# Kernel optimization log

Measured on AMD Instinct MI355X. Metric: run time of the kernel, lower is better.

Reference implementation:

```python
import jax, jax.numpy as jnp
import numpy as np

WS = 7            # window size
HEADS = 4
DIM = 128         # hidden_dim
HEAD_DIM = 128    # wrapper passes head_dim=hidden_dim (faithful to source)
INNER = HEADS * HEAD_DIM   # 512
MLP = 4 * DIM
PATCH = 4
DISP = WS // 2
NEG = -1e9


def _ln(x, g, b, eps=1e-5):
    m = jnp.mean(x, -1, keepdims=True)
    v = jnp.mean((x - m) ** 2, -1, keepdims=True)
    return (x - m) * jax.lax.rsqrt(v + eps) * g + b


_coords = np.stack(np.meshgrid(np.arange(WS), np.arange(WS), indexing='ij'), -1).reshape(-1, 2)
REL_IDX = jnp.asarray(_coords[None] - _coords[:, None] + WS - 1)  # (ws^2, ws^2, 2)


def _build_masks():
    n = WS * WS
    ul = np.zeros((n, n), np.float32)
    ul[-DISP * WS:, : -DISP * WS] = NEG
    ul[: -DISP * WS, -DISP * WS:] = NEG
    lr = np.zeros((WS, WS, WS, WS), np.float32)
    lr[:, -DISP:, :, : -DISP] = NEG
    lr[:, : -DISP, :, -DISP:] = NEG
    return jnp.asarray(ul), jnp.asarray(lr.reshape(n, n))

UL_MASK, LR_MASK = _build_masks()


def _win_attn(x, w_qkv, pos, w_o, b_o, shifted):
    b, H, W, _ = x.shape
    if shifted:
        x = jnp.roll(x, (-DISP, -DISP), axis=(1, 2))
    nh, nw = H // WS, W // WS
    qkv = x @ w_qkv  # (b, H, W, 3*INNER)

    def to_win(t):  # -> (b, heads, n_windows, ws*ws, head_dim)
        t = t.reshape(b, nh, WS, nw, WS, HEADS, HEAD_DIM)
        return t.transpose(0, 5, 1, 3, 2, 4, 6).reshape(b, HEADS, nh * nw, WS * WS, HEAD_DIM)

    q, k, v = map(to_win, jnp.split(qkv, 3, axis=-1))
    dots = jnp.einsum('bhwid,bhwjd->bhwij', q, k) * (HEAD_DIM ** -0.5)
    dots = dots + pos[REL_IDX[..., 0], REL_IDX[..., 1]]  # shared across heads (berniwal)
    if shifted:
        dots = dots.at[:, :, -nw:].add(UL_MASK)
        dots = dots.at[:, :, nw - 1::nw].add(LR_MASK)
    attn = jax.nn.softmax(dots, axis=-1)
    out = jnp.einsum('bhwij,bhwjd->bhwid', attn, v)
    out = out.reshape(b, HEADS, nh, nw, WS, WS, HEAD_DIM).transpose(0, 2, 4, 3, 5, 1, 6)
    out = out.reshape(b, H, W, INNER) @ w_o + b_o
    if shifted:
        out = jnp.roll(out, (DISP, DISP), axis=(1, 2))
    return out


def _block(x, ga1, be1, w_qkv, pos, w_o, b_o, ga2, be2, w1, b1, w2, b2, shifted):
    x = x + _win_attn(_ln(x, ga1, be1), w_qkv, pos, w_o, b_o, shifted)
    h = jax.nn.gelu(_ln(x, ga2, be2) @ w1 + b1, approximate=False) @ w2 + b2
    return x + h


def _patch_embed(x, w, b):  # Unfold(patch) + Linear, channel-major feature order
    B, C, H, W = x.shape
    nh, nw = H // PATCH, W // PATCH
    x = x.reshape(B, C, nh, PATCH, nw, PATCH).transpose(0, 2, 4, 1, 3, 5)
    return x.reshape(B, nh, nw, C * PATCH * PATCH) @ w + b


def setup_inputs() -> dict:
    key = jax.random.key(0)
    ks = iter(jax.random.split(key, 48))

    def nrm(shape, s=0.02):
        return jax.random.normal(next(ks), shape, dtype=jnp.float32) * s

    inp = {'x': jax.random.normal(next(ks), (32, 3, 224, 224), dtype=jnp.float32)}
    inp['w_pe'] = nrm((3 * PATCH * PATCH, DIM))
    inp['b_pe'] = jnp.zeros((DIM,), jnp.float32)
    for s in ('a', 'b'):
        inp['ga1_' + s] = jnp.ones((DIM,), jnp.float32)
        inp['be1_' + s] = jnp.zeros((DIM,), jnp.float32)
        inp['w_qkv_' + s] = nrm((DIM, 3 * INNER))
        inp['pos_' + s] = nrm((2 * WS - 1, 2 * WS - 1), 1.0)
        inp['w_o_' + s] = nrm((INNER, DIM))
        inp['b_o_' + s] = jnp.zeros((DIM,), jnp.float32)
        inp['ga2_' + s] = jnp.ones((DIM,), jnp.float32)
        inp['be2_' + s] = jnp.zeros((DIM,), jnp.float32)
        inp['w_m1_' + s] = nrm((DIM, MLP))
        inp['b_m1_' + s] = jnp.zeros((MLP,), jnp.float32)
        inp['w_m2_' + s] = nrm((MLP, DIM))
        inp['b_m2_' + s] = jnp.zeros((DIM,), jnp.float32)
    return inp


def reference(x, w_pe, b_pe,
              ga1_a, be1_a, w_qkv_a, pos_a, w_o_a, b_o_a, ga2_a, be2_a, w_m1_a, b_m1_a, w_m2_a, b_m2_a,
              ga1_b, be1_b, w_qkv_b, pos_b, w_o_b, b_o_b, ga2_b, be2_b, w_m1_b, b_m1_b, w_m2_b, b_m2_b):
    h = _patch_embed(x, w_pe, b_pe)  # (B, 56, 56, DIM)
    h = _block(h, ga1_a, be1_a, w_qkv_a, pos_a, w_o_a, b_o_a, ga2_a, be2_a, w_m1_a, b_m1_a, w_m2_a, b_m2_a, False)
    h = _block(h, ga1_b, be1_b, w_qkv_b, pos_b, w_o_b, b_o_b, ga2_b, be2_b, w_m1_b, b_m1_b, w_m2_b, b_m2_b, True)
    return h
```

## Files before the change

kernel.cpp:

```cpp
#include <hip/hip_runtime.h>

typedef __attribute__((ext_vector_type(8))) short bf16x8;
typedef __attribute__((ext_vector_type(4))) short bf16x4;
typedef __attribute__((ext_vector_type(4))) float f32x4;
typedef __attribute__((ext_vector_type(2))) unsigned u32x2;

#define MFMA16(a, b, c) __builtin_amdgcn_mfma_f32_16x16x32_bf16(a, b, c, 0, 0, 0)

static __device__ __forceinline__ short f2bf(float f) {
    union { float f; unsigned u; } x; x.f = f;
    unsigned r = x.u + 0x7FFFu + ((x.u >> 16) & 1u);
    return (short)(r >> 16);
}

static __device__ __forceinline__ unsigned cvtpk(float lo, float hi) {
    unsigned r;
    asm("v_cvt_pk_bf16_f32 %0, %1, %2" : "=v"(r) : "v"(lo), "v"(hi));
    return r;
}

static __device__ __forceinline__ void gload16(const void* g, void* l) {
    __builtin_amdgcn_global_load_lds((const __attribute__((address_space(1))) void*)g,
                                     (__attribute__((address_space(3))) void*)l, 16, 0, 0);
}

static __device__ __forceinline__ float gelu(float t) {
    return 0.5f * t * (1.f + erff(t * 0.70710678118f));
}

__global__ void wconv_kernel(const float* __restrict__ i_qkv, const float* __restrict__ i_o,
                             const float* __restrict__ i_m1, const float* __restrict__ i_m2,
                             short* __restrict__ wqkv, short* __restrict__ wo,
                             short* __restrict__ wm1, short* __restrict__ wm2) {
    int idx = blockIdx.x * 256 + threadIdx.x;
    if (idx < 196608) {
        int k = idx & 127, n = idx >> 7;
        wqkv[idx] = f2bf(i_qkv[k * 1536 + n]);
    } else if (idx < 262144) {
        int l = idx - 196608; int k = l & 511, n = l >> 9;
        wo[l] = f2bf(i_o[k * 128 + n]);
    } else if (idx < 327680) {
        int l = idx - 262144; int k = l & 127, n = l >> 7;
        wm1[l] = f2bf(i_m1[k * 512 + n]);
    } else {
        int l = idx - 327680; int k = l & 511, n = l >> 9;
        wm2[l] = f2bf(i_m2[k * 128 + n]);
    }
}

__global__ __launch_bounds__(128) void mtgen_kernel(const float* __restrict__ wqkv,
                                                    short* __restrict__ mt) {
    const int h = blockIdx.x >> 7, e = blockIdx.x & 127;
    __shared__ float s_wk[128];
    const int d = threadIdx.x;
    s_wk[d] = wqkv[(size_t)e * 1536 + 512 + h * 128 + d];
    __syncthreads();
    const float* wq = wqkv + (size_t)d * 1536 + h * 128;
    float acc = 0.f;
#pragma unroll
    for (int o = 0; o < 128; ++o) acc += wq[o] * s_wk[o];
    mt[(size_t)(h * 128 + e) * 128 + d] = f2bf(acc * 0.08838834764831845f);
}

__global__ void tabgen_kernel(const float* __restrict__ pos_a, const float* __restrict__ pos_b,
                              float* __restrict__ tab) {
    int v = blockIdx.x;
    const float* pos = (v == 0) ? pos_a : pos_b;
    for (int e = threadIdx.x; e < 4096; e += 256) {
        int row = e >> 6, key = e & 63;
        float val;
        if (key >= 49) val = -1e9f;
        else if (row >= 49) val = 0.f;
        else {
            int qi = row / 7, qj = row - qi * 7, ki = key / 7, kj = key - ki * 7;
            val = pos[(ki - qi + 6) * 13 + (kj - qj + 6)];
            if (v >= 1) {
                bool wh7 = (v - 1) & 2, ww7 = (v - 1) & 1;
                if (wh7 && ((qi >= 4) != (ki >= 4))) val += -1e9f;
                if (ww7 && ((qj >= 4) != (kj >= 4))) val += -1e9f;
            }
        }
        tab[v * 4096 + e] = val;
    }
}

__global__ __launch_bounds__(256) void patchln_kernel(const float* __restrict__ x,
                                                      const float* __restrict__ w,
                                                      const float* __restrict__ bias,
                                                      const float* __restrict__ g,
                                                      const float* __restrict__ bta,
                                                      float* __restrict__ out,
                                                      short* __restrict__ xn) {
    __shared__ float s_in[2][48];
    __shared__ float red[2][2][2];
    const int tid = threadIdx.x;
    const int half = tid >> 7, c = tid & 127;
    const int winh = (tid >> 6) & 1, lane = tid & 63;
    const int t = blockIdx.x * 2 + half;
    const int b = t / 3136, rem = t - b * 3136;
    const int hp = rem / 56, wp = rem - hp * 56;
    if (c < 48) {
        int cin = c >> 4, py = (c >> 2) & 3, px = c & 3;
        s_in[half][c] = x[((size_t)(b * 3 + cin) * 224 + hp * 4 + py) * 224 + wp * 4 + px];
    }
    __syncthreads();
    float acc = bias[c];
#pragma unroll
    for (int k = 0; k < 48; ++k) acc += s_in[half][k] * w[k * 128 + c];
    out[(size_t)t * 128 + c] = acc;
    float s1 = acc, s2 = acc * acc;
#pragma unroll
    for (int o = 32; o > 0; o >>= 1) { s1 += __shfl_xor(s1, o); s2 += __shfl_xor(s2, o); }
    if (lane == 0) { red[half][winh][0] = s1; red[half][winh][1] = s2; }
    __syncthreads();
    s1 = red[half][0][0] + red[half][1][0];
    s2 = red[half][0][1] + red[half][1][1];
    float mean = s1 * (1.f / 128.f);
    float var = s2 * (1.f / 128.f) - mean * mean;
    float rstd = rsqrtf(var + 1e-5f);
    xn[(size_t)t * 128 + c] = f2bf((acc - mean) * rstd * g[c] + bta[c]);
}

template <int SHIFTED>
__global__ __launch_bounds__(256, 3) void attn_kernel(const short* __restrict__ xn,
                                                      const short* __restrict__ wqkvT,
                                                      const short* __restrict__ mt,
                                                      const float* __restrict__ tab,
                                                      const short* __restrict__ zpad,
                                                      short* __restrict__ aout) {
    __shared__ short smem[24576];
    short* s_x = smem;
    short* s_T = smem + 8192;
    short* s_v = smem + 16384;
    short* s_p = smem;

    const int tid = threadIdx.x;
    const int wid = tid >> 6, lane = tid & 63;
    const int l15 = lane & 15, l4 = lane >> 4, klo = l4 * 8;
    const int bid = blockIdx.x;
    const int win = bid & 63, head = (bid >> 6) & 3, b = bid >> 8;
    const int wh = win >> 3, ww = win & 7;

#pragma unroll
    for (int it = 0; it < 4; ++it) {
        int slot = it * 256 + tid;
        int row = slot >> 4, scol = slot & 15;
        int colb = (scol * 16) ^ ((row & 7) << 4);
        const char* g;
        if (row < 49) {
            int wi = (row * 37) >> 8, wj = row - wi * 7;
            int hh = wh * 7 + wi, wp = ww * 7 + wj;
            if (SHIFTED) { hh += 3; if (hh >= 56) hh -= 56; wp += 3; if (wp >= 56) wp -= 56; }
            int t = (b * 56 + hh) * 56 + wp;
            g = (const char*)(xn + (size_t)t * 128) + colb;
        } else {
            g = (const char*)zpad + colb;
        }
        gload16(g, (char*)smem + (it * 256 + wid * 64) * 16);
    }
    __syncthreads();

    const f32x4 zero4 = {0.f, 0.f, 0.f, 0.f};

    {
        const short* Mh = mt + (size_t)head * 16384;
        const short* Wv = wqkvT + (size_t)(1024 + head * 128) * 128;
        f32x4 at[2][4], av[4][2];
#pragma unroll
        for (int mw = 0; mw < 2; ++mw)
#pragma unroll
            for (int j = 0; j < 4; ++j) at[mw][j] = zero4;
#pragma unroll
        for (int m = 0; m < 4; ++m)
#pragma unroll
            for (int n = 0; n < 2; ++n) av[m][n] = zero4;
#pragma unroll
        for (int k0 = 0; k0 < 4; ++k0) {
            bf16x8 bx[4], awt[2], bwv[2];
#pragma unroll
            for (int j = 0; j < 4; ++j) {
                int row = j * 16 + l15;
                bx[j] = *(const bf16x8*)((const char*)s_x + row * 256 + ((k0 * 64 + l4 * 16) ^ ((row & 7) << 4)));
            }
#pragma unroll
            for (int mw = 0; mw < 2; ++mw)
                awt[mw] = *(const bf16x8*)(Mh + (size_t)(wid * 32 + mw * 16 + l15) * 128 + k0 * 32 + klo);
#pragma unroll
            for (int n = 0; n < 2; ++n)
                bwv[n] = *(const bf16x8*)(Wv + (size_t)(wid * 32 + n * 16 + l15) * 128 + k0 * 32 + klo);
            __builtin_amdgcn_s_setprio(1);
#pragma unroll
            for (int mw = 0; mw < 2; ++mw)
#pragma unroll
                for (int j = 0; j < 4; ++j) at[mw][j] = MFMA16(awt[mw], bx[j], at[mw][j]);
#pragma unroll
            for (int m = 0; m < 4; ++m)
#pragma unroll
                for (int n = 0; n < 2; ++n) av[m][n] = MFMA16(bx[m], bwv[n], av[m][n]);
            __builtin_amdgcn_s_setprio(0);
        }
#pragma unroll
        for (int mw = 0; mw < 2; ++mw)
#pragma unroll
            for (int j = 0; j < 4; ++j) {
                u32x2 pq = { cvtpk(at[mw][j][0], at[mw][j][1]), cvtpk(at[mw][j][2], at[mw][j][3]) };
                int row = j * 16 + l15;
                *(u32x2*)((char*)s_T + row * 256 + ((wid * 64 + mw * 32 + l4 * 8) ^ ((row & 7) << 4))) = pq;
            }
#pragma unroll
        for (int m = 0; m < 4; ++m)
#pragma unroll
            for (int n = 0; n < 2; ++n) {
                u32x2 pv = { cvtpk(av[m][n][0], av[m][n][1]), cvtpk(av[m][n][2], av[m][n][3]) };
                int hd = wid * 32 + n * 16 + l15;
                *(u32x2*)((char*)s_v + hd * 128 + ((m * 32 + l4 * 8) ^ ((hd & 7) << 4))) = pv;
            }
    }
    __syncthreads();

    const int qrow = wid * 16 + l15;
    f32x4 dt[4];
#pragma unroll
    for (int m = 0; m < 4; ++m) dt[m] = zero4;
#pragma unroll
    for (int k0 = 0; k0 < 4; ++k0) {
        bf16x8 bq = *(const bf16x8*)((const char*)s_T + qrow * 256 + ((k0 * 64 + l4 * 16) ^ ((qrow & 7) << 4)));
        __builtin_amdgcn_s_setprio(1);
#pragma unroll
        for (int m = 0; m < 4; ++m) {
            int krow = m * 16 + l15;
            bf16x8 akf = *(const bf16x8*)((const char*)s_x + krow * 256 + ((k0 * 64 + l4 * 16) ^ ((krow & 7) << 4)));
            dt[m] = MFMA16(akf, bq, dt[m]);
        }
        __builtin_amdgcn_s_setprio(0);
    }
    __syncthreads();

    const int variant = SHIFTED ? (1 + ((wh == 7) ? 2 : 0) + ((ww == 7) ? 1 : 0)) : 0;
    const float* tv = tab + variant * 4096 + qrow * 64;
    float p[4][4];
    float mx = -3.0e38f;
#pragma unroll
    for (int m = 0; m < 4; ++m) {
        f32x4 tb = *(const f32x4*)(tv + m * 16 + l4 * 4);
#pragma unroll
        for (int r = 0; r < 4; ++r) {
            float d = dt[m][r] + tb[r];
            p[m][r] = d;
            mx = fmaxf(mx, d);
        }
    }
    mx = fmaxf(mx, __shfl_xor(mx, 16));
    mx = fmaxf(mx, __shfl_xor(mx, 32));
    float sum = 0.f;
#pragma unroll
    for (int m = 0; m < 4; ++m)
#pragma unroll
        for (int r = 0; r < 4; ++r) { p[m][r] = __expf(p[m][r] - mx); sum += p[m][r]; }
    sum += __shfl_xor(sum, 16);
    sum += __shfl_xor(sum, 32);
    float inv = 1.f / sum;
#pragma unroll
    for (int m = 0; m < 4; ++m) {
        u32x2 pv = { cvtpk(p[m][0] * inv, p[m][1] * inv), cvtpk(p[m][2] * inv, p[m][3] * inv) };
        *(u32x2*)((char*)s_p + qrow * 128 + ((m * 32 + l4 * 8) ^ ((qrow & 7) << 4))) = pv;
    }
    __syncthreads();

    f32x4 o[4][2];
#pragma unroll
    for (int m = 0; m < 4; ++m)
#pragma unroll
        for (int n = 0; n < 2; ++n) o[m][n] = zero4;
#pragma unroll
    for (int k0 = 0; k0 < 2; ++k0) {
        bf16x8 ap[4], bv[2];
#pragma unroll
        for (int m = 0; m < 4; ++m) {
            int row = m * 16 + l15;
            ap[m] = *(const bf16x8*)((const char*)s_p + row * 128 + ((k0 * 64 + l4 * 16) ^ ((row & 7) << 4)));
        }
#pragma unroll
        for (int n = 0; n < 2; ++n) {
            int hd = wid * 32 + n * 16 + l15;
            bv[n] = *(const bf16x8*)((const char*)s_v + hd * 128 + ((k0 * 64 + l4 * 16) ^ ((hd & 7) << 4)));
        }
        __builtin_amdgcn_s_setprio(1);
#pragma unroll
        for (int m = 0; m < 4; ++m)
#pragma unroll
            for (int n = 0; n < 2; ++n) o[m][n] = MFMA16(ap[m], bv[n], o[m][n]);
        __builtin_amdgcn_s_setprio(0);
    }
#pragma unroll
    for (int m = 0; m < 4; ++m) {
#pragma unroll
        for (int r = 0; r < 4; ++r) {
            int rl = m * 16 + l4 * 4 + r;
            if (rl < 49) {
                int wi = (rl * 37) >> 8, wj = rl - wi * 7;
                int hh = wh * 7 + wi, wp = ww * 7 + wj;
                if (SHIFTED) { hh += 3; if (hh >= 56) hh -= 56; wp += 3; if (wp >= 56) wp -= 56; }
                size_t t = (size_t)(b * 56 + hh) * 56 + wp;
                aout[t * 512 + head * 128 + wid * 32 + l15] = f2bf(o[m][0][r]);
                aout[t * 512 + head * 128 + wid * 32 + 16 + l15] = f2bf(o[m][1][r]);
            }
        }
    }
}

__global__ __launch_bounds__(256, 2) void projmlp_kernel(const short* __restrict__ A,
                                                         const short* __restrict__ woT,
                                                         const short* __restrict__ wm1T,
                                                         const float* __restrict__ b_o,
                                                         const float* __restrict__ ga2,
                                                         const float* __restrict__ be2,
                                                         const float* __restrict__ b1,
                                                         float* __restrict__ outf,
                                                         short* __restrict__ hid) {
    __shared__ char smem[65536];
    float* red = (float*)(smem + 32768);

    const int tid = threadIdx.x, wid = tid >> 6, lane = tid & 63;
    const int wr = wid >> 1, wc = wid & 1;
    const int l15 = lane & 15, l4 = lane >> 4;
    const int m0 = blockIdx.x * 128;

    auto stage = [&](int kc, int bi) {
#pragma unroll
        for (int it = 0; it < 4; ++it) {
            int slot = it * 256 + tid;
            int row = slot >> 3, scol = slot & 7;
            int colb = (scol * 16) ^ ((row & 7) << 4);
            gload16((const char*)(A + (size_t)(m0 + row) * 512 + kc * 64) + colb,
                    (char*)smem + bi * 32768 + (it * 256 + wid * 64) * 16);
        }
#pragma unroll
        for (int it = 0; it < 4; ++it) {
            int slot = it * 256 + tid;
            int row = slot >> 3, scol = slot & 7;
            int colb = (scol * 16) ^ ((row & 7) << 4);
            gload16((const char*)(woT + (size_t)row * 512 + kc * 64) + colb,
                    (char*)smem + bi * 32768 + 16384 + (it * 256 + wid * 64) * 16);
        }
    };

    const f32x4 zero4 = {0.f, 0.f, 0.f, 0.f};
    f32x4 acc[4][4];
#pragma unroll
    for (int nf = 0; nf < 4; ++nf)
#pragma unroll
        for (int tm = 0; tm < 4; ++tm) acc[nf][tm] = zero4;

    stage(0, 0);
    __syncthreads();
#pragma unroll
    for (int kc = 0; kc < 8; ++kc) {
        if (kc + 1 < 8) stage(kc + 1, (kc + 1) & 1);
        const char* bufA = (const char*)smem + (kc & 1) * 32768;
        const char* bufB = bufA + 16384;
#pragma unroll
        for (int ks = 0; ks < 2; ++ks) {
            bf16x8 a[4], bfr[4];
#pragma unroll
            for (int tm = 0; tm < 4; ++tm) {
                int row = wr * 64 + tm * 16 + l15;
                a[tm] = *(const bf16x8*)(bufA + row * 128 + ((ks * 64 + l4 * 16) ^ ((row & 7) << 4)));
            }
#pragma unroll
            for (int nf = 0; nf < 4; ++nf) {
                int row = wc * 64 + nf * 16 + l15;
                bfr[nf] = *(const bf16x8*)(bufB + row * 128 + ((ks * 64 + l4 * 16) ^ ((row & 7) << 4)));
            }
            __builtin_amdgcn_s_setprio(1);
#pragma unroll
            for (int nf = 0; nf < 4; ++nf)
#pragma unroll
                for (int tm = 0; tm < 4; ++tm) acc[nf][tm] = MFMA16(bfr[nf], a[tm], acc[nf][tm]);
            __builtin_amdgcn_s_setprio(0);
        }
        __syncthreads();
    }

    f32x4 bv4[4];
#pragma unroll
    for (int nf = 0; nf < 4; ++nf)
        bv4[nf] = *(const f32x4*)(b_o + wc * 64 + nf * 16 + l4 * 4);

    float s1[4], s2[4];
#pragma unroll
    for (int tm = 0; tm < 4; ++tm) {
        int row = m0 + wr * 64 + tm * 16 + l15;
        float a1 = 0.f, a2 = 0.f;
#pragma unroll
        for (int nf = 0; nf < 4; ++nf) {
            f32x4 rs = *(const f32x4*)(outf + (size_t)row * 128 + wc * 64 + nf * 16 + l4 * 4);
#pragma unroll
            for (int r = 0; r < 4; ++r) {
                float v = acc[nf][tm][r] + bv4[nf][r] + rs[r];
                acc[nf][tm][r] = v;
                a1 += v; a2 += v * v;
            }
        }
        s1[tm] = a1; s2[tm] = a2;
    }
#pragma unroll
    for (int tm = 0; tm < 4; ++tm) {
        s1[tm] += __shfl_xor(s1[tm], 16); s1[tm] += __shfl_xor(s1[tm], 32);
        s2[tm] += __shfl_xor(s2[tm], 16); s2[tm] += __shfl_xor(s2[tm], 32);
    }
    if (l4 == 0) {
#pragma unroll
        for (int tm = 0; tm < 4; ++tm) {
            int lrow = wr * 64 + tm * 16 + l15;
            red[lrow * 4 + wc * 2] = s1[tm];
            red[lrow * 4 + wc * 2 + 1] = s2[tm];
        }
    }
    __syncthreads();

    float mean[4], rstd[4];
#pragma unroll
    for (int tm = 0; tm < 4; ++tm) {
        int lrow = wr * 64 + tm * 16 + l15;
        f32x4 rd = *(const f32x4*)(red + lrow * 4);
        float t1 = rd[0] + rd[2], t2 = rd[1] + rd[3];
        mean[tm] = t1 * (1.f / 128.f);
        float var = t2 * (1.f / 128.f) - mean[tm] * mean[tm];
        rstd[tm] = rsqrtf(var + 1e-5f);
    }
    __syncthreads();

#pragma unroll
    for (int tm = 0; tm < 4; ++tm) {
        int lrow = wr * 64 + tm * 16 + l15;
        int row = m0 + lrow;
#pragma unroll
        for (int nf = 0; nf < 4; ++nf) {
            int col0 = wc * 64 + nf * 16 + l4 * 4;
            *(f32x4*)(outf + (size_t)row * 128 + col0) = acc[nf][tm];
            f32x4 gg = *(const f32x4*)(ga2 + col0);
            f32x4 bb = *(const f32x4*)(be2 + col0);
            float w0 = (acc[nf][tm][0] - mean[tm]) * rstd[tm] * gg[0] + bb[0];
            float w1 = (acc[nf][tm][1] - mean[tm]) * rstd[tm] * gg[1] + bb[1];
            float w2 = (acc[nf][tm][2] - mean[tm]) * rstd[tm] * gg[2] + bb[2];
            float w3 = (acc[nf][tm][3] - mean[tm]) * rstd[tm] * gg[3] + bb[3];
            u32x2 pb = { cvtpk(w0, w1), cvtpk(w2, w3) };
            *(u32x2*)((char*)smem + lrow * 256 + ((col0 * 2) ^ ((lrow & 7) << 4))) = pb;
        }
    }
    __syncthreads();

    for (int hc = 0; hc < 4; ++hc) {
#pragma unroll
        for (int it = 0; it < 8; ++it) {
            int slot = it * 256 + tid;
            int row = slot >> 4, scol = slot & 15;
            int colb = (scol * 16) ^ ((row & 7) << 4);
            gload16((const char*)(wm1T + (size_t)(hc * 128 + row) * 128) + colb,
                    (char*)smem + 32768 + (it * 256 + wid * 64) * 16);
        }
        __syncthreads();

        f32x4 acc2[4][4];
#pragma unroll
        for (int nf = 0; nf < 4; ++nf)
#pragma unroll
            for (int tm = 0; tm < 4; ++tm) acc2[nf][tm] = zero4;
#pragma unroll
        for (int ks = 0; ks < 4; ++ks) {
            bf16x8 a[4], bfr[4];
#pragma unroll
            for (int tm = 0; tm < 4; ++tm) {
                int row = wr * 64 + tm * 16 + l15;
                a[tm] = *(const bf16x8*)((const char*)smem + row * 256 + ((ks * 64 + l4 * 16) ^ ((row & 7) << 4)));
            }
#pragma unroll
            for (int nf = 0; nf < 4; ++nf) {
                int hrow = wc * 64 + nf * 16 + l15;
                bfr[nf] = *(const bf16x8*)((const char*)smem + 32768 + hrow * 256 + ((ks * 64 + l4 * 16) ^ ((hrow & 7) << 4)));
            }
            __builtin_amdgcn_s_setprio(1);
#pragma unroll
            for (int nf = 0; nf < 4; ++nf)
#pragma unroll
                for (int tm = 0; tm < 4; ++tm) acc2[nf][tm] = MFMA16(bfr[nf], a[tm], acc2[nf][tm]);
            __builtin_amdgcn_s_setprio(0);
        }

        f32x4 b14[4];
#pragma unroll
        for (int nf = 0; nf < 4; ++nf)
            b14[nf] = *(const f32x4*)(b1 + hc * 128 + wc * 64 + nf * 16 + l4 * 4);
#pragma unroll
        for (int tm = 0; tm < 4; ++tm) {
            int row = m0 + wr * 64 + tm * 16 + l15;
#pragma unroll
            for (int nf = 0; nf < 4; ++nf) {
                float v0 = gelu(acc2[nf][tm][0] + b14[nf][0]);
                float v1 = gelu(acc2[nf][tm][1] + b14[nf][1]);
                float v2 = gelu(acc2[nf][tm][2] + b14[nf][2]);
                float v3 = gelu(acc2[nf][tm][3] + b14[nf][3]);
                u32x2 pv = { cvtpk(v0, v1), cvtpk(v2, v3) };
                *(u32x2*)(hid + (size_t)row * 512 + hc * 128 + wc * 64 + nf * 16 + l4 * 4) = pv;
            }
        }
        __syncthreads();
    }
}

template <int MODE>
__global__ __launch_bounds__(256, 2) void gemm4_kernel(const short* __restrict__ A,
                                                       const short* __restrict__ BT,
                                                       const float* __restrict__ bias,
                                                       const float* __restrict__ g,
                                                       const float* __restrict__ bta,
                                                       float* __restrict__ outf,
                                                       short* __restrict__ outb) {
    __shared__ char smem[65536];
    float* red = (float*)smem;

    const int tid = threadIdx.x, wid = tid >> 6, lane = tid & 63;
    const int wr = wid >> 1, wc = wid & 1;
    const int l15 = lane & 15, l4 = lane >> 4;
    const int m0 = blockIdx.x * 128;

    auto stage = [&](int kc, int bi) {
#pragma unroll
        for (int it = 0; it < 4; ++it) {
            int slot = it * 256 + tid;
            int row = slot >> 3, scol = slot & 7;
            int colb = (scol * 16) ^ ((row & 7) << 4);
            gload16((const char*)(A + (size_t)(m0 + row) * 512 + kc * 64) + colb,
                    (char*)smem + bi * 32768 + (it * 256 + wid * 64) * 16);
        }
#pragma unroll
        for (int it = 0; it < 4; ++it) {
            int slot = it * 256 + tid;
            int row = slot >> 3, scol = slot & 7;
            int colb = (scol * 16) ^ ((row & 7) << 4);
            gload16((const char*)(BT + (size_t)row * 512 + kc * 64) + colb,
                    (char*)smem + bi * 32768 + 16384 + (it * 256 + wid * 64) * 16);
        }
    };

    const f32x4 zero4 = {0.f, 0.f, 0.f, 0.f};
    f32x4 acc[4][4];
#pragma unroll
    for (int nf = 0; nf < 4; ++nf)
#pragma unroll
        for (int tm = 0; tm < 4; ++tm) acc[nf][tm] = zero4;

    stage(0, 0);
    __syncthreads();
#pragma unroll
    for (int kc = 0; kc < 8; ++kc) {
        if (kc + 1 < 8) stage(kc + 1, (kc + 1) & 1);
        const char* bufA = (const char*)smem + (kc & 1) * 32768;
        const char* bufB = bufA + 16384;
#pragma unroll
        for (int ks = 0; ks < 2; ++ks) {
            bf16x8 a[4], bfr[4];
#pragma unroll
            for (int tm = 0; tm < 4; ++tm) {
                int row = wr * 64 + tm * 16 + l15;
                a[tm] = *(const bf16x8*)(bufA + row * 128 + ((ks * 64 + l4 * 16) ^ ((row & 7) << 4)));
            }
#pragma unroll
            for (int nf = 0; nf < 4; ++nf) {
                int row = wc * 64 + nf * 16 + l15;
                bfr[nf] = *(const bf16x8*)(bufB + row * 128 + ((ks * 64 + l4 * 16) ^ ((row & 7) << 4)));
            }
            __builtin_amdgcn_s_setprio(1);
#pragma unroll
            for (int nf = 0; nf < 4; ++nf)
#pragma unroll
                for (int tm = 0; tm < 4; ++tm) acc[nf][tm] = MFMA16(bfr[nf], a[tm], acc[nf][tm]);
            __builtin_amdgcn_s_setprio(0);
        }
        __syncthreads();
    }

    f32x4 bv4[4];
#pragma unroll
    for (int nf = 0; nf < 4; ++nf)
        bv4[nf] = *(const f32x4*)(bias + wc * 64 + nf * 16 + l4 * 4);

    float s1[4], s2[4];
#pragma unroll
    for (int tm = 0; tm < 4; ++tm) {
        int row = m0 + wr * 64 + tm * 16 + l15;
        float a1 = 0.f, a2 = 0.f;
#pragma unroll
        for (int nf = 0; nf < 4; ++nf) {
            f32x4 rs = *(const f32x4*)(outf + (size_t)row * 128 + wc * 64 + nf * 16 + l4 * 4);
#pragma unroll
            for (int r = 0; r < 4; ++r) {
                float v = acc[nf][tm][r] + bv4[nf][r] + rs[r];
                acc[nf][tm][r] = v;
                a1 += v; a2 += v * v;
            }
        }
        s1[tm] = a1; s2[tm] = a2;
    }

    if (MODE == 1) {
#pragma unroll
        for (int tm = 0; tm < 4; ++tm) {
            s1[tm] += __shfl_xor(s1[tm], 16); s1[tm] += __shfl_xor(s1[tm], 32);
            s2[tm] += __shfl_xor(s2[tm], 16); s2[tm] += __shfl_xor(s2[tm], 32);
        }
        if (l4 == 0) {
#pragma unroll
            for (int tm = 0; tm < 4; ++tm) {
                int lrow = wr * 64 + tm * 16 + l15;
                red[lrow * 4 + wc * 2] = s1[tm];
                red[lrow * 4 + wc * 2 + 1] = s2[tm];
            }
        }
        __syncthreads();
    }

#pragma unroll
    for (int tm = 0; tm < 4; ++tm) {
        int lrow = wr * 64 + tm * 16 + l15;
        int row = m0 + lrow;
        float mean = 0.f, rstd = 0.f;
        if (MODE == 1) {
            f32x4 rd = *(const f32x4*)(red + lrow * 4);
            float t1 = rd[0] + rd[2], t2 = rd[1] + rd[3];
            mean = t1 * (1.f / 128.f);
            float var = t2 * (1.f / 128.f) - mean * mean;
            rstd = rsqrtf(var + 1e-5f);
        }
#pragma unroll
        for (int nf = 0; nf < 4; ++nf) {
            int col0 = wc * 64 + nf * 16 + l4 * 4;
            *(f32x4*)(outf + (size_t)row * 128 + col0) = acc[nf][tm];
            if (MODE == 1) {
                f32x4 gg = *(const f32x4*)(g + col0);
                f32x4 bb = *(const f32x4*)(bta + col0);
                float w0 = (acc[nf][tm][0] - mean) * rstd * gg[0] + bb[0];
                float w1 = (acc[nf][tm][1] - mean) * rstd * gg[1] + bb[1];
                float w2 = (acc[nf][tm][2] - mean) * rstd * gg[2] + bb[2];
                float w3 = (acc[nf][tm][3] - mean) * rstd * gg[3] + bb[3];
                u32x2 pb = { cvtpk(w0, w1), cvtpk(w2, w3) };
                *(u32x2*)(outb + (size_t)row * 128 + col0) = pb;
            }
        }
    }
}

extern "C" void kernel_launch(void* const* d_in, const int* in_sizes, int n_in,
                              void* d_out, int out_size, void* d_ws, size_t ws_size,
                              hipStream_t stream) {
    const float* x = (const float*)d_in[0];
    const float* w_pe = (const float*)d_in[1];
    const float* b_pe = (const float*)d_in[2];
    const float* P[24];
    for (int i = 0; i < 24; ++i) P[i] = (const float*)d_in[3 + i];

    float* out = (float*)d_out;
    const size_t TOK = 100352;

    short* xn = (short*)d_ws;
    short* abuf = xn + TOK * 128;
    short* wqkv = abuf + TOK * 512;
    short* wo = wqkv + 196608;
    short* wm1 = wo + 65536;
    short* wm2 = wm1 + 65536;
    short* mtb = wm2 + 65536;
    float* tab = (float*)(mtb + 65536);
    short* zpad = (short*)(tab + 5 * 4096);

    hipMemsetAsync(zpad, 0, 256, stream);
    tabgen_kernel<<<5, 256, 0, stream>>>(P[3], P[15], tab);

    patchln_kernel<<<50176, 256, 0, stream>>>(x, w_pe, b_pe, P[0], P[1], out, xn);

    for (int s = 0; s < 2; ++s) {
        wconv_kernel<<<1536, 256, 0, stream>>>(P[s * 12 + 2], P[s * 12 + 4], P[s * 12 + 8], P[s * 12 + 10],
                                               wqkv, wo, wm1, wm2);
        mtgen_kernel<<<512, 128, 0, stream>>>(P[s * 12 + 2], mtb);

        if (s == 0)
            attn_kernel<0><<<8192, 256, 0, stream>>>(xn, wqkv, mtb, tab, zpad, abuf);
        else
            attn_kernel<1><<<8192, 256, 0, stream>>>(xn, wqkv, mtb, tab, zpad, abuf);

        projmlp_kernel<<<784, 256, 0, stream>>>(
            abuf, wo, wm1, P[s * 12 + 5], P[s * 12 + 6], P[s * 12 + 7], P[s * 12 + 9], out, abuf);

        if (s == 0)
            gemm4_kernel<1><<<784, 256, 0, stream>>>(
                abuf, wm2, P[11], P[12], P[13], out, xn);
        else
            gemm4_kernel<2><<<784, 256, 0, stream>>>(
                abuf, wm2, P[23], nullptr, nullptr, out, nullptr);
    }
}
```

Before: 549.9 us.

## Vectorize attention output stores, clamp pad rows, load gemm4 weights directly from global

```diff
diff --git a/kernel.cpp b/kernel.cpp
--- a/kernel.cpp
+++ b/kernel.cpp
@@ -126,7 +126,6 @@
                                                       const short* __restrict__ wqkvT,
                                                       const short* __restrict__ mt,
                                                       const float* __restrict__ tab,
-                                                      const short* __restrict__ zpad,
                                                       short* __restrict__ aout) {
     __shared__ short smem[24576];
     short* s_x = smem;
@@ -141,22 +140,28 @@
     const int win = bid & 63, head = (bid >> 6) & 3, b = bid >> 8;
     const int wh = win >> 3, ww = win & 7;
 
+    int trow[4];
+#pragma unroll
+    for (int j = 0; j < 4; ++j) {
+        int r = j * 16 + l15; r = (r > 48) ? 48 : r;
+        int wi = (r * 37) >> 8, wj = r - wi * 7;
+        int hh = wh * 7 + wi, wp = ww * 7 + wj;
+        if (SHIFTED) { hh += 3; if (hh >= 56) hh -= 56; wp += 3; if (wp >= 56) wp -= 56; }
+        trow[j] = (b * 56 + hh) * 56 + wp;
+    }
+
 #pragma unroll
     for (int it = 0; it < 4; ++it) {
         int slot = it * 256 + tid;
         int row = slot >> 4, scol = slot & 15;
         int colb = (scol * 16) ^ ((row & 7) << 4);
-        const char* g;
-        if (row < 49) {
-            int wi = (row * 37) >> 8, wj = row - wi * 7;
-            int hh = wh * 7 + wi, wp = ww * 7 + wj;
-            if (SHIFTED) { hh += 3; if (hh >= 56) hh -= 56; wp += 3; if (wp >= 56) wp -= 56; }
-            int t = (b * 56 + hh) * 56 + wp;
-            g = (const char*)(xn + (size_t)t * 128) + colb;
-        } else {
-            g = (const char*)zpad + colb;
-        }
-        gload16(g, (char*)smem + (it * 256 + wid * 64) * 16);
+        int rr = (row > 48) ? 48 : row;
+        int wi = (rr * 37) >> 8, wj = rr - wi * 7;
+        int hh = wh * 7 + wi, wp = ww * 7 + wj;
+        if (SHIFTED) { hh += 3; if (hh >= 56) hh -= 56; wp += 3; if (wp >= 56) wp -= 56; }
+        int t = (b * 56 + hh) * 56 + wp;
+        gload16((const char*)(xn + (size_t)t * 128) + colb,
+                (char*)smem + (it * 256 + wid * 64) * 16);
     }
     __syncthreads();
 
@@ -267,43 +272,39 @@
     }
     __syncthreads();
 
-    f32x4 o[4][2];
-#pragma unroll
-    for (int m = 0; m < 4; ++m)
-#pragma unroll
-        for (int n = 0; n < 2; ++n) o[m][n] = zero4;
+    f32x4 o[2][4];
+#pragma unroll
+    for (int fn = 0; fn < 2; ++fn)
+#pragma unroll
+        for (int tm = 0; tm < 4; ++tm) o[fn][tm] = zero4;
 #pragma unroll
     for (int k0 = 0; k0 < 2; ++k0) {
-        bf16x8 ap[4], bv[2];
-#pragma unroll
-        for (int m = 0; m < 4; ++m) {
-            int row = m * 16 + l15;
-            ap[m] = *(const bf16x8*)((const char*)s_p + row * 128 + ((k0 * 64 + l4 * 16) ^ ((row & 7) << 4)));
-        }
-#pragma unroll
-        for (int n = 0; n < 2; ++n) {
-            int hd = wid * 32 + n * 16 + l15;
-            bv[n] = *(const bf16x8*)((const char*)s_v + hd * 128 + ((k0 * 64 + l4 * 16) ^ ((hd & 7) << 4)));
+        bf16x8 ap[4], bv2[2];
+#pragma unroll
+        for (int tm = 0; tm < 4; ++tm) {
+            int row = tm * 16 + l15;
+            ap[tm] = *(const bf16x8*)((const char*)s_p + row * 128 + ((k0 * 64 + l4 * 16) ^ ((row & 7) << 4)));
+        }
+#pragma unroll
+        for (int fn = 0; fn < 2; ++fn) {
+            int hd = wid * 32 + fn * 16 + l15;
+            bv2[fn] = *(const bf16x8*)((const char*)s_v + hd * 128 + ((k0 * 64 + l4 * 16) ^ ((hd & 7) << 4)));
         }
         __builtin_amdgcn_s_setprio(1);
 #pragma unroll
-        for (int m = 0; m < 4; ++m)
-#pragma unroll
-            for (int n = 0; n < 2; ++n) o[m][n] = MFMA16(ap[m], bv[n], o[m][n]);
+        for (int fn = 0; fn < 2; ++fn)
+#pragma unroll
+            for (int tm = 0; tm < 4; ++tm) o[fn][tm] = MFMA16(bv2[fn], ap[tm], o[fn][tm]);
         __builtin_amdgcn_s_setprio(0);
     }
 #pragma unroll
-    for (int m = 0; m < 4; ++m) {
-#pragma unroll
-        for (int r = 0; r < 4; ++r) {
-            int rl = m * 16 + l4 * 4 + r;
-            if (rl < 49) {
-                int wi = (rl * 37) >> 8, wj = rl - wi * 7;
-                int hh = wh * 7 + wi, wp = ww * 7 + wj;
-                if (SHIFTED) { hh += 3; if (hh >= 56) hh -= 56; wp += 3; if (wp >= 56) wp -= 56; }
-                size_t t = (size_t)(b * 56 + hh) * 56 + wp;
-                aout[t * 512 + head * 128 + wid * 32 + l15] = f2bf(o[m][0][r]);
-                aout[t * 512 + head * 128 + wid * 32 + 16 + l15] = f2bf(o[m][1][r]);
+    for (int tm = 0; tm < 4; ++tm) {
+        if (tm * 16 + l15 < 49) {
+            short* dst = aout + (size_t)trow[tm] * 512 + head * 128 + wid * 32 + l4 * 4;
+#pragma unroll
+            for (int fn = 0; fn < 2; ++fn) {
+                u32x2 pv = { cvtpk(o[fn][tm][0], o[fn][tm][1]), cvtpk(o[fn][tm][2], o[fn][tm][3]) };
+                *(u32x2*)(dst + fn * 16) = pv;
             }
         }
     }
@@ -510,19 +511,19 @@
 }
 
 template <int MODE>
-__global__ __launch_bounds__(256, 2) void gemm4_kernel(const short* __restrict__ A,
+__global__ __launch_bounds__(256, 3) void gemm4_kernel(const short* __restrict__ A,
                                                        const short* __restrict__ BT,
                                                        const float* __restrict__ bias,
                                                        const float* __restrict__ g,
                                                        const float* __restrict__ bta,
                                                        float* __restrict__ outf,
                                                        short* __restrict__ outb) {
-    __shared__ char smem[65536];
+    __shared__ char smem[32768];
     float* red = (float*)smem;
 
     const int tid = threadIdx.x, wid = tid >> 6, lane = tid & 63;
     const int wr = wid >> 1, wc = wid & 1;
-    const int l15 = lane & 15, l4 = lane >> 4;
+    const int l15 = lane & 15, l4 = lane >> 4, klo = l4 * 8;
     const int m0 = blockIdx.x * 128;
 
     auto stage = [&](int kc, int bi) {
@@ -532,15 +533,7 @@
             int row = slot >> 3, scol = slot & 7;
             int colb = (scol * 16) ^ ((row & 7) << 4);
             gload16((const char*)(A + (size_t)(m0 + row) * 512 + kc * 64) + colb,
-                    (char*)smem + bi * 32768 + (it * 256 + wid * 64) * 16);
-        }
-#pragma unroll
-        for (int it = 0; it < 4; ++it) {
-            int slot = it * 256 + tid;
-            int row = slot >> 3, scol = slot & 7;
-            int colb = (scol * 16) ^ ((row & 7) << 4);
-            gload16((const char*)(BT + (size_t)row * 512 + kc * 64) + colb,
-                    (char*)smem + bi * 32768 + 16384 + (it * 256 + wid * 64) * 16);
+                    (char*)smem + bi * 16384 + (it * 256 + wid * 64) * 16);
         }
     };
 
@@ -556,26 +549,26 @@
 #pragma unroll
     for (int kc = 0; kc < 8; ++kc) {
         if (kc + 1 < 8) stage(kc + 1, (kc + 1) & 1);
-        const char* bufA = (const char*)smem + (kc & 1) * 32768;
-        const char* bufB = bufA + 16384;
+        bf16x8 bfr[2][4];
+#pragma unroll
+        for (int ks = 0; ks < 2; ++ks)
+#pragma unroll
+            for (int nf = 0; nf < 4; ++nf)
+                bfr[ks][nf] = *(const bf16x8*)(BT + (size_t)(wc * 64 + nf * 16 + l15) * 512 + kc * 64 + ks * 32 + klo);
+        const char* bufA = (const char*)smem + (kc & 1) * 16384;
 #pragma unroll
         for (int ks = 0; ks < 2; ++ks) {
-            bf16x8 a[4], bfr[4];
+            bf16x8 a[4];
 #pragma unroll
             for (int tm = 0; tm < 4; ++tm) {
                 int row = wr * 64 + tm * 16 + l15;
                 a[tm] = *(const bf16x8*)(bufA + row * 128 + ((ks * 64 + l4 * 16) ^ ((row & 7) << 4)));
             }
-#pragma unroll
-            for (int nf = 0; nf < 4; ++nf) {
-                int row = wc * 64 + nf * 16 + l15;
-                bfr[nf] = *(const bf16x8*)(bufB + row * 128 + ((ks * 64 + l4 * 16) ^ ((row & 7) << 4)));
-            }
             __builtin_amdgcn_s_setprio(1);
 #pragma unroll
             for (int nf = 0; nf < 4; ++nf)
 #pragma unroll
-                for (int tm = 0; tm < 4; ++tm) acc[nf][tm] = MFMA16(bfr[nf], a[tm], acc[nf][tm]);
+                for (int tm = 0; tm < 4; ++tm) acc[nf][tm] = MFMA16(bfr[ks][nf], a[tm], acc[nf][tm]);
             __builtin_amdgcn_s_setprio(0);
         }
         __syncthreads();
@@ -671,9 +664,7 @@
     short* wm2 = wm1 + 65536;
     short* mtb = wm2 + 65536;
     float* tab = (float*)(mtb + 65536);
-    short* zpad = (short*)(tab + 5 * 4096);
-
-    hipMemsetAsync(zpad, 0, 256, stream);
+
     tabgen_kernel<<<5, 256, 0, stream>>>(P[3], P[15], tab);
 
     patchln_kernel<<<50176, 256, 0, stream>>>(x, w_pe, b_pe, P[0], P[1], out, xn);
@@ -684,9 +675,9 @@
         mtgen_kernel<<<512, 128, 0, stream>>>(P[s * 12 + 2], mtb);
 
         if (s == 0)
-            attn_kernel<0><<<8192, 256, 0, stream>>>(xn, wqkv, mtb, tab, zpad, abuf);
+            attn_kernel<0><<<8192, 256, 0, stream>>>(xn, wqkv, mtb, tab, abuf);
         else
-            attn_kernel<1><<<8192, 256, 0, stream>>>(xn, wqkv, mtb, tab, zpad, abuf);
+            attn_kernel<1><<<8192, 256, 0, stream>>>(xn, wqkv, mtb, tab, abuf);
 
         projmlp_kernel<<<784, 256, 0, stream>>>(
             abuf, wo, wm1, P[s * 12 + 5], P[s * 12 + 6], P[s * 12 + 7], P[s * 12 + 9], out, abuf);
```

Result: slower. 598.4 us (+8.8%).
